# Performance work log

Measured on AMD Instinct MI355X. Metric: run time of the kernel, lower is better.

The kernel has to match this reference:

```python
import jax, jax.numpy as jnp
import numpy as np

N_HEADS = 8
TOPK = 32


def setup_inputs() -> dict:
    key = jax.random.key(0)
    ks = jax.random.split(key, 6)
    N, L, Hd = 2, 2048, 512
    s = 1.0 / np.sqrt(Hd).astype(np.float32)
    return {
        "queries": jax.random.normal(ks[0], (N, L, Hd), jnp.float32),
        "keys": jax.random.normal(ks[1], (N, L, Hd), jnp.float32),
        "values": jax.random.normal(ks[2], (N, L, Hd), jnp.float32),
        "Wq": jax.random.normal(ks[3], (Hd, Hd), jnp.float32) * s,
        "bq": jnp.zeros((Hd,), jnp.float32),
        "Wk": jax.random.normal(ks[4], (Hd, Hd), jnp.float32) * s,
        "bk": jnp.zeros((Hd,), jnp.float32),
        "Wv": jax.random.normal(ks[5], (Hd, Hd), jnp.float32) * s,
        "bv": jnp.zeros((Hd,), jnp.float32),
    }


def reference(queries, keys, values, Wq, bq, Wk, bk, Wv, bv):
    N, L, Hd = queries.shape
    S = keys.shape[1]
    H = N_HEADS
    E = Hd // H
    q = (queries @ Wq.T + bq).reshape(N, L, H, E)
    k = (keys @ Wk.T + bk).reshape(N, S, H, E)
    v = (values @ Wv.T + bv).reshape(N, S, H, E)
    temp = 1.0 / np.sqrt(E).astype(np.float32)
    QK = jnp.einsum("nlhe,nshe->nhls", q, k)  # [N,H,L,S]
    topk = min(TOPK, S)
    _, idx = jax.lax.top_k(QK, topk)  # idx: [N,H,L,topk]
    ni = jnp.arange(N)[:, None, None, None]
    hi = jnp.arange(H)[None, :, None, None]
    li = jnp.arange(L)[None, None, :, None]
    keep = jnp.zeros(QK.shape, bool).at[ni, hi, li, idx].set(True)
    # torch: softmax(temp * (QK + mask)) with mask 0 on top-k, -inf elsewhere
    scores = jnp.where(keep, temp * QK, -jnp.inf)
    A = jax.nn.softmax(scores, axis=-1)  # dropout is identity in eval mode
    V = jnp.einsum("nhls,nshd->nlhd", A, v).reshape(N, L, Hd)
    return V, A
```

## Files before the change

kernel.cpp:

```cpp
#include <hip/hip_runtime.h>
#include <cstdint>
#include <cstddef>
#include <math.h>

#define NH     8
#define EH     64
#define HD     512
#define NBATCH 2
#define LSEQ   2048
#define TK     32


using f32x4  = __attribute__((ext_vector_type(4))) float;
using bf16x8 = __attribute__((ext_vector_type(8))) short;
using u16x8  = __attribute__((ext_vector_type(8))) unsigned short;
using u16x4  = __attribute__((ext_vector_type(4))) unsigned short;

#define A_TOTAL4 16777216ull
#define PROJ_THREADS 393216ull

__device__ __forceinline__ unsigned short f2b(float f) {
    unsigned u = __float_as_uint(f);
    return (unsigned short)((u + 0x7FFFu + ((u >> 16) & 1u)) >> 16);
}
__device__ __forceinline__ unsigned f2key(float f) {
    unsigned u = __float_as_uint(f);
    return (u & 0x80000000u) ? ~u : (u | 0x80000000u);
}
__device__ __forceinline__ float key2f(unsigned k) {
    return __uint_as_float((k & 0x80000000u) ? (k ^ 0x80000000u) : ~k);
}
__device__ __forceinline__ unsigned umax2(unsigned a, unsigned b) { return a > b ? a : b; }

__global__ __launch_bounds__(256) void proj_kernel(
    const float* __restrict__ Xq, const float* __restrict__ Xk, const float* __restrict__ Xv,
    const float* __restrict__ Wq, const float* __restrict__ Bq,
    const float* __restrict__ Wk, const float* __restrict__ Bk,
    const float* __restrict__ Wv, const float* __restrict__ Bv,
    float* __restrict__ ws, float* __restrict__ outA)
{
    const int z = blockIdx.z;
    const float* X = (z == 0) ? Xq : (z == 1) ? Xk : Xv;
    const float* W = (z == 0) ? Wq : (z == 1) ? Wk : Wv;
    const float* B = (z == 0) ? Bq : (z == 1) ? Bk : Bv;
    float* out = ws + (size_t)z * 2097152;
    unsigned short* khi = (unsigned short*)(ws + 6291456);

    __shared__ float4 Xs[64 * 8];
    __shared__ float4 Ws[64 * 8];
    __shared__ unsigned short kst[64 * 72];

    const int tid = threadIdx.x;
    const int tx = tid & 15, ty = tid >> 4;
    const int m0 = blockIdx.x * 64, n0 = blockIdx.y * 64;
    const int lin = (blockIdx.z * gridDim.y + blockIdx.y) * gridDim.x + blockIdx.x;
    const size_t gtid = (size_t)lin * 256 + tid;
    float4* outA4 = (float4*)outA;
    const float4 z4 = make_float4(0.f, 0.f, 0.f, 0.f);

    float acc[4][4];
    #pragma unroll
    for (int i = 0; i < 4; ++i)
        #pragma unroll
        for (int j = 0; j < 4; ++j) acc[i][j] = 0.f;

    int cc = 0;
    for (int k0 = 0; k0 < HD; k0 += 32, ++cc) {
        #pragma unroll
        for (int it = 0; it < 2; ++it) {
            int f = tid + it * 256;
            int row = f >> 3, c = f & 7;
            int cs = c ^ ((row >> 2) & 7);
            Xs[row * 8 + cs] = *(const float4*)&X[(size_t)(m0 + row) * HD + k0 + c * 4];
            Ws[row * 8 + cs] = *(const float4*)&W[(size_t)(n0 + row) * HD + k0 + c * 4];
        }
        #pragma unroll
        for (int j = 0; j < 3; ++j) {
            size_t zi = gtid + (size_t)(cc * 3 + j) * PROJ_THREADS;
            if (zi < A_TOTAL4) outA4[zi] = z4;
        }
        __syncthreads();
        #pragma unroll
        for (int c = 0; c < 8; ++c) {
            float4 av[4], bv4[4];
            #pragma unroll
            for (int i = 0; i < 4; ++i) { int r = ty * 4 + i; av[i]  = Xs[r * 8 + (c ^ ((r >> 2) & 7))]; }
            #pragma unroll
            for (int j = 0; j < 4; ++j) { int r = tx * 4 + j; bv4[j] = Ws[r * 8 + (c ^ ((r >> 2) & 7))]; }
            #pragma unroll
            for (int i = 0; i < 4; ++i)
                #pragma unroll
                for (int j = 0; j < 4; ++j) {
                    acc[i][j] = fmaf(av[i].x, bv4[j].x, acc[i][j]);
                    acc[i][j] = fmaf(av[i].y, bv4[j].y, acc[i][j]);
                    acc[i][j] = fmaf(av[i].z, bv4[j].z, acc[i][j]);
                    acc[i][j] = fmaf(av[i].w, bv4[j].w, acc[i][j]);
                }
        }
        __syncthreads();
    }

    #pragma unroll
    for (int j = 0; j < 4; ++j) {
        int o = n0 + tx * 4 + j;
        float bb = B[o];
        int h = o >> 6, e = o & 63;
        #pragma unroll
        for (int i = 0; i < 4; ++i) {
            int m = m0 + ty * 4 + i;
            int n = m >> 11, s = m & 2047;
            float val = acc[i][j] + bb;
            int head = n * NH + h;
            out[(size_t)head * 131072 + (size_t)s * EH + e] = val;
            if (z == 1) kst[(ty * 4 + i) * 72 + e] = f2b(val);
        }
    }

    if (z == 1) {
        __syncthreads();
        const int head = (m0 >> 11) * NH + (n0 >> 6);
        const int kt0  = (m0 & 2047) >> 4;
        #pragma unroll
        for (int it = 0; it < 2; ++it) {
            int g = tid + it * 256;
            int lane_g = g & 63;
            int rest = g >> 6;
            int kt = rest >> 1, ksb = rest & 1;
            int s_loc = kt * 16 + (lane_g & 15);
            int e0 = ksb * 32 + ((lane_g >> 4) << 3);
            u16x8 vv = *(const u16x8*)&kst[s_loc * 72 + e0];
            size_t idx = ((((size_t)head * 128 + (kt0 + kt)) * 2 + ksb) * 64 + lane_g) * 8;
            *(u16x8*)&khi[idx] = vv;
        }
    }
}

__device__ __forceinline__ unsigned long long sort64_desc(unsigned long long v, int lane) {
    #pragma unroll
    for (int k = 2; k <= 64; k <<= 1)
        #pragma unroll
        for (int j = k >> 1; j >= 1; j >>= 1) {
            unsigned long long o = __shfl_xor(v, j, 64);
            bool up = ((lane & k) != 0);
            bool keepmin = (((lane & j) == 0) == up);
            unsigned long long lo = v < o ? v : o;
            unsigned long long hi = v > o ? v : o;
            v = keepmin ? lo : hi;
        }
    return v;
}
__device__ __forceinline__ unsigned long long merge_top64(unsigned long long a, unsigned long long b, int lane) {
    unsigned long long br = __shfl(b, 63 - lane, 64);
    unsigned long long m = a > br ? a : br;
    #pragma unroll
    for (int j = 32; j >= 1; j >>= 1) {
        unsigned long long o = __shfl_xor(m, j, 64);
        bool keepmax = ((lane & j) == 0);
        unsigned long long mx = m > o ? m : o;
        unsigned long long mn = m < o ? m : o;
        m = keepmax ? mx : mn;
    }
    return m;
}

__global__ __launch_bounds__(512, 4) void attn_kernel(
    const float* __restrict__ ws, float* __restrict__ outV, float* __restrict__ outA)
{
    const float* qw = ws;
    const float* kw = ws + 2097152;
    const float* vw = ws + 4194304;
    const unsigned short* khi = (const unsigned short*)(ws + 6291456);

    __shared__ unsigned short scores16[2048 * 16];
    __shared__ float qs[EH * 16];
    __shared__ unsigned short candArr[8 * 256];

    const int tid  = threadIdx.x;
    const int lane = tid & 63;
    const int uwv  = __builtin_amdgcn_readfirstlane(tid) >> 6;

    unsigned bid = blockIdx.x;
    unsigned id  = (bid & 7u) * 256u + (bid >> 3);
    const int head = (int)(id >> 7);
    const int l0   = (int)(id & 127u) * 16;
    const size_t headoff = (size_t)head * 131072;

    #pragma unroll
    for (int it = 0; it < 2; ++it) {
        int i = tid + it * 512;
        int row = i & 15, e = i >> 4;
        qs[i] = qw[headoff + (size_t)(l0 + row) * EH + e];
    }
    __syncthreads();

    {
        bf16x8 afrag[2];
        #pragma unroll
        for (int ks = 0; ks < 2; ++ks)
            #pragma unroll
            for (int j = 0; j < 8; ++j) {
                int e = ks * 32 + ((lane >> 4) << 3) + j;
                afrag[ks][j] = (short)f2b(qs[e * 16 + (lane & 15)]);
            }

        #pragma unroll
        for (int kt = 0; kt < 16; ++kt) {
            f32x4 acc = (f32x4)(0.f);
            int ktg = uwv * 16 + kt;
            #pragma unroll
            for (int ks = 0; ks < 2; ++ks) {
                bf16x8 b = *(const bf16x8*)(khi + (size_t)head * 131072 +
                              ((((size_t)ktg * 2 + ks) * 64 + lane) << 3));
                acc = __builtin_amdgcn_mfma_f32_16x16x32_bf16(afrag[ks], b, acc, 0, 0, 0);
            }
            int key = uwv * 256 + kt * 16 + (lane & 15);
            int rbase = (lane >> 4) << 2;
            int p = rbase ^ (key & 12);
            u16x4 s4;
            #pragma unroll
            for (int reg = 0; reg < 4; ++reg)
                s4[reg] = (unsigned short)(f2key(acc[reg]) >> 16);
            *(u16x4*)&scores16[key * 16 + p] = s4;
        }
    }
    __syncthreads();

    unsigned short* cand = candArr + uwv * 256;
    const unsigned long long lmlt = (1ull << lane) - 1ull;
    int selS[2]; float selW[2];

    const int r0 = 2 * uwv;
    unsigned pk[32];
    #pragma unroll
    for (int t = 0; t < 32; ++t) {
        int key = t * 64 + lane;
        int p0 = r0 ^ (key & 12);
        pk[t] = *(const unsigned*)&scores16[key * 16 + p0];
    }

    #pragma unroll
    for (int rr2 = 0; rr2 < 2; ++rr2) {
        const int lrow = l0 + r0 + rr2;

        unsigned mx = 0;
        #pragma unroll
        for (int t = 0; t < 32; ++t) {
            unsigned a = rr2 ? (pk[t] >> 16) : (pk[t] & 0xFFFFu);
            mx = umax2(mx, a);
        }
        {
            unsigned v = mx;
            #pragma unroll
            for (int k = 2; k <= 64; k <<= 1)
                #pragma unroll
                for (int j = k >> 1; j >= 1; j >>= 1) {
                    unsigned o = __shfl_xor(v, j);
                    bool up = ((lane & k) == 0);
                    bool keepmin = (((lane & j) == 0) == up);
                    unsigned lo = v < o ? v : o, hi = v > o ? v : o;
                    v = keepmin ? lo : hi;
                }
            mx = __shfl(v, 32);
        }
        const unsigned tau16 = mx;
        const float tauf = key2f(tau16 << 16);
        const unsigned thr16 = f2key(tauf - 0.35f) >> 16;

        int Nc = 0;
        #pragma unroll
        for (int t = 0; t < 32; ++t) {
            unsigned a = rr2 ? (pk[t] >> 16) : (pk[t] & 0xFFFFu);
            bool c = a >= thr16;
            unsigned long long b = __ballot(c);
            if (c) {
                int p = Nc + __popcll(b & lmlt);
                if (p < 256) cand[p] = (unsigned short)(t * 64 + lane);
            }
            Nc += __popcll(b);
        }
        if (Nc > 256) Nc = 256;
        const int nch = (Nc + 63) >> 6;

        const float* qrow = qw + headoff + (size_t)lrow * EH;
        float4 qv[16];
        #pragma unroll
        for (int c4 = 0; c4 < 16; ++c4) qv[c4] = *(const float4*)&qrow[c4 * 4];

        unsigned long long best = 0ull;
        for (int c = 0; c < nch; ++c) {
            int p = c * 64 + lane;
            bool valid = p < Nc;
            int si = valid ? (int)cand[p] : 0;
            const float* krow = kw + headoff + (size_t)si * EH;
            float sc = 0.f;
            #pragma unroll
            for (int c4 = 0; c4 < 16; ++c4) {
                float4 kv = *(const float4*)&krow[c4 * 4];
                sc = fmaf(qv[c4].x, kv.x, sc);
                sc = fmaf(qv[c4].y, kv.y, sc);
                sc = fmaf(qv[c4].z, kv.z, sc);
                sc = fmaf(qv[c4].w, kv.w, sc);
            }
            unsigned long long comp = valid
                ? ((((unsigned long long)f2key(sc)) << 32) | (unsigned)(~si))
                : 0ull;
            comp = sort64_desc(comp, lane);
            best = (c == 0) ? comp : merge_top64(best, comp, lane);
        }

        unsigned key32 = (unsigned)(best >> 32);
        int si = (int)(~((unsigned)best)) & 2047;
        float sc = key2f(key32);
        float M = __shfl(sc, 0);
        float ee = (lane < TK) ? __expf(0.125f * (sc - M)) : 0.f;
        float Z = ee;
        #pragma unroll
        for (int d = 1; d < 64; d <<= 1) Z += __shfl_xor(Z, d);
        selS[rr2] = si;
        selW[rr2] = ee / Z;
    }

    #pragma unroll
    for (int rr2 = 0; rr2 < 2; ++rr2) {
        const int lrow = l0 + r0 + rr2;
        float* Arow = outA + ((size_t)head * 2048 + lrow) * 2048;
        if (lane < TK) Arow[selS[rr2]] = selW[rr2];

        float acc = 0.f;
        int   siv = selS[rr2];
        unsigned wbits = __float_as_uint(selW[rr2]);
        #pragma unroll
        for (int i = 0; i < TK; ++i) {
            int s_i   = __builtin_amdgcn_readlane(siv, i);
            float w_i = __uint_as_float((unsigned)__builtin_amdgcn_readlane((int)wbits, i));
            acc = fmaf(w_i, vw[headoff + (size_t)s_i * EH + lane], acc);
        }
        const int n = head >> 3, h = head & 7;
        outV[((size_t)(n * 2048 + lrow)) * 512 + h * 64 + lane] = acc;
    }
}

extern "C" void kernel_launch(void* const* d_in, const int* in_sizes, int n_in,
                              void* d_out, int out_size, void* d_ws, size_t ws_size,
                              hipStream_t stream)
{
    (void)in_sizes; (void)n_in; (void)out_size; (void)ws_size;
    const float* q  = (const float*)d_in[0];
    const float* k  = (const float*)d_in[1];
    const float* v  = (const float*)d_in[2];
    const float* Wq = (const float*)d_in[3];
    const float* bq = (const float*)d_in[4];
    const float* Wk = (const float*)d_in[5];
    const float* bk = (const float*)d_in[6];
    const float* Wv = (const float*)d_in[7];
    const float* bv = (const float*)d_in[8];
    float* ws   = (float*)d_ws;
    float* outV = (float*)d_out;
    float* outA = outV + (size_t)NBATCH * LSEQ * HD;

    proj_kernel<<<dim3(64, 8, 3), 256, 0, stream>>>(q, k, v, Wq, bq, Wk, bk, Wv, bv, ws, outA);
    attn_kernel<<<dim3(2048, 1, 1), 512, 0, stream>>>(ws, outV, outA);
}
```

Baseline: 233.3 us.

## Build dense attention rows in LDS and widen projection tile to 64x128

The zero-fill of the 128 MB attention matrix moves out of the projection kernel. Each attention wave now builds its full 2048-float row in shared memory (reusing the score buffer behind an added barrier), scatters the top-k weights into it, and writes the row with coalesced float4 stores instead of a separate zero pass followed by scattered writes. The projection GEMM tile grows to 64x128 per block with 4x8 accumulators, float4 epilogue stores, a new swizzle for the larger W tile, and launch bounds set to 3 blocks. The goal is to write the A output once and raise arithmetic intensity, at the cost of extra LDS traffic per row and more registers in the projection kernel.

```diff
diff --git a/kernel.cpp b/kernel.cpp
--- a/kernel.cpp
+++ b/kernel.cpp
@@ -16,9 +16,6 @@
 using u16x8  = __attribute__((ext_vector_type(8))) unsigned short;
 using u16x4  = __attribute__((ext_vector_type(4))) unsigned short;
 
-#define A_TOTAL4 16777216ull
-#define PROJ_THREADS 393216ull
-
 __device__ __forceinline__ unsigned short f2b(float f) {
     unsigned u = __float_as_uint(f);
     return (unsigned short)((u + 0x7FFFu + ((u >> 16) & 1u)) >> 16);
@@ -31,13 +28,15 @@
     return __uint_as_float((k & 0x80000000u) ? (k ^ 0x80000000u) : ~k);
 }
 __device__ __forceinline__ unsigned umax2(unsigned a, unsigned b) { return a > b ? a : b; }
-
-__global__ __launch_bounds__(256) void proj_kernel(
+__device__ __forceinline__ int swzA(int r, int c) { return c ^ ((r >> 2) & 7); }
+__device__ __forceinline__ int swzB(int r, int c) { return c ^ (((r >> 2) ^ (r >> 5)) & 7); }
+
+__global__ __launch_bounds__(256, 3) void proj_kernel(
     const float* __restrict__ Xq, const float* __restrict__ Xk, const float* __restrict__ Xv,
     const float* __restrict__ Wq, const float* __restrict__ Bq,
     const float* __restrict__ Wk, const float* __restrict__ Bk,
     const float* __restrict__ Wv, const float* __restrict__ Bv,
-    float* __restrict__ ws, float* __restrict__ outA)
+    float* __restrict__ ws)
 {
     const int z = blockIdx.z;
     const float* X = (z == 0) ? Xq : (z == 1) ? Xk : Xv;
@@ -47,89 +46,93 @@
     unsigned short* khi = (unsigned short*)(ws + 6291456);
 
     __shared__ float4 Xs[64 * 8];
-    __shared__ float4 Ws[64 * 8];
-    __shared__ unsigned short kst[64 * 72];
+    __shared__ float4 Ws[128 * 8];
+    __shared__ unsigned short kst[64 * 136];
 
     const int tid = threadIdx.x;
     const int tx = tid & 15, ty = tid >> 4;
-    const int m0 = blockIdx.x * 64, n0 = blockIdx.y * 64;
-    const int lin = (blockIdx.z * gridDim.y + blockIdx.y) * gridDim.x + blockIdx.x;
-    const size_t gtid = (size_t)lin * 256 + tid;
-    float4* outA4 = (float4*)outA;
-    const float4 z4 = make_float4(0.f, 0.f, 0.f, 0.f);
-
-    float acc[4][4];
+    const int m0 = blockIdx.x * 64, n0 = blockIdx.y * 128;
+
+    float acc[4][8];
     #pragma unroll
     for (int i = 0; i < 4; ++i)
         #pragma unroll
-        for (int j = 0; j < 4; ++j) acc[i][j] = 0.f;
-
-    int cc = 0;
-    for (int k0 = 0; k0 < HD; k0 += 32, ++cc) {
+        for (int j = 0; j < 8; ++j) acc[i][j] = 0.f;
+
+    for (int k0 = 0; k0 < HD; k0 += 32) {
         #pragma unroll
         for (int it = 0; it < 2; ++it) {
             int f = tid + it * 256;
             int row = f >> 3, c = f & 7;
-            int cs = c ^ ((row >> 2) & 7);
-            Xs[row * 8 + cs] = *(const float4*)&X[(size_t)(m0 + row) * HD + k0 + c * 4];
-            Ws[row * 8 + cs] = *(const float4*)&W[(size_t)(n0 + row) * HD + k0 + c * 4];
-        }
-        #pragma unroll
-        for (int j = 0; j < 3; ++j) {
-            size_t zi = gtid + (size_t)(cc * 3 + j) * PROJ_THREADS;
-            if (zi < A_TOTAL4) outA4[zi] = z4;
+            Xs[row * 8 + swzA(row, c)] = *(const float4*)&X[(size_t)(m0 + row) * HD + k0 + c * 4];
+        }
+        #pragma unroll
+        for (int it = 0; it < 4; ++it) {
+            int f = tid + it * 256;
+            int row = f >> 3, c = f & 7;
+            Ws[row * 8 + swzB(row, c)] = *(const float4*)&W[(size_t)(n0 + row) * HD + k0 + c * 4];
         }
         __syncthreads();
         #pragma unroll
         for (int c = 0; c < 8; ++c) {
-            float4 av[4], bv4[4];
-            #pragma unroll
-            for (int i = 0; i < 4; ++i) { int r = ty * 4 + i; av[i]  = Xs[r * 8 + (c ^ ((r >> 2) & 7))]; }
-            #pragma unroll
-            for (int j = 0; j < 4; ++j) { int r = tx * 4 + j; bv4[j] = Ws[r * 8 + (c ^ ((r >> 2) & 7))]; }
+            float4 av[4], bv[8];
+            #pragma unroll
+            for (int i = 0; i < 4; ++i) { int r = ty * 4 + i; av[i] = Xs[r * 8 + swzA(r, c)]; }
+            #pragma unroll
+            for (int j = 0; j < 8; ++j) { int r = tx * 8 + j; bv[j] = Ws[r * 8 + swzB(r, c)]; }
             #pragma unroll
             for (int i = 0; i < 4; ++i)
                 #pragma unroll
-                for (int j = 0; j < 4; ++j) {
-                    acc[i][j] = fmaf(av[i].x, bv4[j].x, acc[i][j]);
-                    acc[i][j] = fmaf(av[i].y, bv4[j].y, acc[i][j]);
-                    acc[i][j] = fmaf(av[i].z, bv4[j].z, acc[i][j]);
-                    acc[i][j] = fmaf(av[i].w, bv4[j].w, acc[i][j]);
+                for (int j = 0; j < 8; ++j) {
+                    acc[i][j] = fmaf(av[i].x, bv[j].x, acc[i][j]);
+                    acc[i][j] = fmaf(av[i].y, bv[j].y, acc[i][j]);
+                    acc[i][j] = fmaf(av[i].z, bv[j].z, acc[i][j]);
+                    acc[i][j] = fmaf(av[i].w, bv[j].w, acc[i][j]);
                 }
         }
         __syncthreads();
     }
 
-    #pragma unroll
-    for (int j = 0; j < 4; ++j) {
-        int o = n0 + tx * 4 + j;
-        float bb = B[o];
-        int h = o >> 6, e = o & 63;
-        #pragma unroll
-        for (int i = 0; i < 4; ++i) {
-            int m = m0 + ty * 4 + i;
-            int n = m >> 11, s = m & 2047;
-            float val = acc[i][j] + bb;
-            int head = n * NH + h;
-            out[(size_t)head * 131072 + (size_t)s * EH + e] = val;
-            if (z == 1) kst[(ty * 4 + i) * 72 + e] = f2b(val);
+    float4 bb[2];
+    bb[0] = *(const float4*)&B[n0 + tx * 8 + 0];
+    bb[1] = *(const float4*)&B[n0 + tx * 8 + 4];
+    #pragma unroll
+    for (int i = 0; i < 4; ++i) {
+        int m = m0 + ty * 4 + i;
+        int n = m >> 11, s = m & 2047;
+        #pragma unroll
+        for (int jj = 0; jj < 2; ++jj) {
+            int o0 = n0 + tx * 8 + jj * 4;
+            int head = n * NH + (o0 >> 6), e0 = o0 & 63;
+            float4 val;
+            val.x = acc[i][jj * 4 + 0] + bb[jj].x;
+            val.y = acc[i][jj * 4 + 1] + bb[jj].y;
+            val.z = acc[i][jj * 4 + 2] + bb[jj].z;
+            val.w = acc[i][jj * 4 + 3] + bb[jj].w;
+            *(float4*)&out[(size_t)head * 131072 + (size_t)s * EH + e0] = val;
+            if (z == 1) {
+                u16x4 b4;
+                b4[0] = f2b(val.x); b4[1] = f2b(val.y);
+                b4[2] = f2b(val.z); b4[3] = f2b(val.w);
+                *(u16x4*)&kst[(ty * 4 + i) * 136 + tx * 8 + jj * 4] = b4;
+            }
         }
     }
 
     if (z == 1) {
         __syncthreads();
-        const int head = (m0 >> 11) * NH + (n0 >> 6);
-        const int kt0  = (m0 & 2047) >> 4;
-        #pragma unroll
-        for (int it = 0; it < 2; ++it) {
+        const int base_head = (m0 >> 11) * NH + (n0 >> 6);
+        const int kt0 = (m0 & 2047) >> 4;
+        #pragma unroll
+        for (int it = 0; it < 4; ++it) {
             int g = tid + it * 256;
             int lane_g = g & 63;
             int rest = g >> 6;
-            int kt = rest >> 1, ksb = rest & 1;
+            int head_loc = rest >> 3, ksb = (rest >> 2) & 1, kt = rest & 3;
             int s_loc = kt * 16 + (lane_g & 15);
-            int e0 = ksb * 32 + ((lane_g >> 4) << 3);
-            u16x8 vv = *(const u16x8*)&kst[s_loc * 72 + e0];
-            size_t idx = ((((size_t)head * 128 + (kt0 + kt)) * 2 + ksb) * 64 + lane_g) * 8;
+            int ecol = head_loc * 64 + ksb * 32 + ((lane_g >> 4) << 3);
+            u16x8 vv = *(const u16x8*)&kst[s_loc * 136 + ecol];
+            size_t idx = ((((size_t)(base_head + head_loc) * 128 + (kt0 + kt)) * 2 + ksb) * 64 + lane_g) * 8;
             *(u16x8*)&khi[idx] = vv;
         }
     }
@@ -237,6 +240,7 @@
         int p0 = r0 ^ (key & 12);
         pk[t] = *(const unsigned*)&scores16[key * 16 + p0];
     }
+    __syncthreads();
 
     #pragma unroll
     for (int rr2 = 0; rr2 < 2; ++rr2) {
@@ -320,11 +324,19 @@
         selW[rr2] = ee / Z;
     }
 
+    float* abuf = (float*)((char*)scores16 + uwv * 8192);
     #pragma unroll
     for (int rr2 = 0; rr2 < 2; ++rr2) {
         const int lrow = l0 + r0 + rr2;
+        float4* ab4 = (float4*)abuf;
+        const float4 z4 = make_float4(0.f, 0.f, 0.f, 0.f);
+        #pragma unroll
+        for (int u = 0; u < 8; ++u) ab4[u * 64 + lane] = z4;
+        if (lane < TK) abuf[selS[rr2]] = selW[rr2];
         float* Arow = outA + ((size_t)head * 2048 + lrow) * 2048;
-        if (lane < TK) Arow[selS[rr2]] = selW[rr2];
+        #pragma unroll
+        for (int u = 0; u < 8; ++u)
+            *(float4*)&Arow[(u * 64 + lane) * 4] = ab4[u * 64 + lane];
 
         float acc = 0.f;
         int   siv = selS[rr2];
@@ -358,6 +370,6 @@
     float* outV = (float*)d_out;
     float* outA = outV + (size_t)NBATCH * LSEQ * HD;
 
-    proj_kernel<<<dim3(64, 8, 3), 256, 0, stream>>>(q, k, v, Wq, bq, Wk, bk, Wv, bv, ws, outA);
+    proj_kernel<<<dim3(64, 4, 3), 256, 0, stream>>>(q, k, v, Wq, bq, Wk, bk, Wv, bv, ws);
     attn_kernel<<<dim3(2048, 1, 1), 512, 0, stream>>>(ws, outV, outA);
 }
```

Measured after the change: 224.5 us. 3.8% less time.
